# Kernel optimization log

Measured on AMD Instinct MI355X. Metric: run time of the kernel, lower is better.

The kernel has to match this reference:

```python
import jax, jax.numpy as jnp
import numpy as np

B, T, HID = 8, 4, 2048
H, HKV, D = 32, 8, 64   # query heads, kv heads, head_dim
S = 8192                # cached kv length
EPS = 1e-6
SCALE = D ** -0.5


def _rmsnorm(x, w, eps=EPS):
    xf = x.astype(jnp.float32)
    var = jnp.mean(xf * xf, axis=-1, keepdims=True)
    return w * (xf * jax.lax.rsqrt(var + eps)).astype(x.dtype)


def _rotate_half(x):
    half = x.shape[-1] // 2
    return jnp.concatenate([-x[..., half:], x[..., :half]], axis=-1)


def setup_inputs() -> dict:
    key = jax.random.key(0)
    ks = jax.random.split(key, 12)
    f = jnp.float32
    x = jax.random.normal(ks[0], (B, T, HID), f)
    theta = jax.random.uniform(ks[1], (B, T, D), f, 0.0, 2.0 * np.pi)
    cos = jnp.cos(theta)
    sin = jnp.sin(theta)
    cache_keys = jax.random.normal(ks[2], (B, HKV, S, D), f) * 0.5
    cache_values = jax.random.normal(ks[3], (B, HKV, S, D), f) * 0.5
    wq = jax.random.normal(ks[4], (HID, H * D), f) * 0.02
    wk = jax.random.normal(ks[5], (HID, HKV * D), f) * 0.02
    wv = jax.random.normal(ks[6], (HID, HKV * D), f) * 0.02
    wo = jax.random.normal(ks[7], (H * D, HID), f) * 0.02
    q_norm_w = jnp.ones((D,), f)
    k_norm_w = jnp.ones((D,), f)
    return {"x": x, "cos": cos, "sin": sin, "cache_keys": cache_keys,
            "cache_values": cache_values, "wq": wq, "wk": wk, "wv": wv,
            "wo": wo, "q_norm_w": q_norm_w, "k_norm_w": k_norm_w}


def reference(x, cos, sin, cache_keys, cache_values, wq, wk, wv, wo, q_norm_w, k_norm_w):
    b, t, _ = x.shape
    # projections + per-head RMSNorm on q/k -> [B,H,T,D]
    q = _rmsnorm((x @ wq).reshape(b, t, H, D), q_norm_w).transpose(0, 2, 1, 3)
    k = _rmsnorm((x @ wk).reshape(b, t, HKV, D), k_norm_w).transpose(0, 2, 1, 3)
    v = (x @ wv).reshape(b, t, HKV, D).transpose(0, 2, 1, 3)
    # RoPE (GPT-NeoX style), cos/sin broadcast over heads
    c = cos[:, None]  # [B,1,T,D]
    s = sin[:, None]
    q = q * c + _rotate_half(q) * s
    k = k * c + _rotate_half(k) * s
    # KV-cache concat along seq dim
    k_full = jnp.concatenate([cache_keys, k], axis=2)   # [B,HKV,S+T,D]
    v_full = jnp.concatenate([cache_values, v], axis=2)
    # GQA attention without materializing repeated KV heads:
    n_rep = H // HKV
    qg = q.reshape(b, HKV, n_rep, t, D)                 # [B,G,R,T,D]
    scores = jnp.einsum('bgrtd,bgsd->bgrts', qg, k_full) * SCALE
    p = jax.nn.softmax(scores, axis=-1)                 # cache present -> no causal mask
    og = jnp.einsum('bgrts,bgsd->bgrtd', p, v_full)
    out = og.reshape(b, H, t, D).transpose(0, 2, 1, 3).reshape(b, t, H * D) @ wo
    return (out, k_full, v_full)
```

## Files before the change

### kernel.cpp

```cpp
#include <hip/hip_runtime.h>
#include <math.h>

#define B 8
#define T 4
#define HID 2048
#define H 32
#define HKV 8
#define D 64
#define S 8192
#define ST (S + T)
#define NREP (H / HKV)
#define EPS 1e-6f
#define SCALE 0.125f

#define SCB 256
#define NSUB 4
#define SUB 64
#define NCB 33
#define NCAT 3072

typedef __attribute__((ext_vector_type(8))) _Float16 half8;
typedef __attribute__((ext_vector_type(4))) _Float16 half4;
typedef __attribute__((ext_vector_type(4))) float f32x4;

#define LGKM_BARRIER()                                                   \
    do {                                                                 \
        asm volatile("s_waitcnt lgkmcnt(0)" ::: "memory");               \
        __builtin_amdgcn_s_barrier();                                    \
        __builtin_amdgcn_sched_barrier(0);                               \
    } while (0)

static __device__ __forceinline__ half8 cvt8(const float4 a, const float4 b) {
    half8 f;
    f[0] = (_Float16)a.x; f[1] = (_Float16)a.y; f[2] = (_Float16)a.z; f[3] = (_Float16)a.w;
    f[4] = (_Float16)b.x; f[5] = (_Float16)b.y; f[6] = (_Float16)b.z; f[7] = (_Float16)b.w;
    return f;
}
static __device__ __forceinline__ half4 cvt4v(const f32x4 a) {
    half4 f;
    f[0] = (_Float16)a[0]; f[1] = (_Float16)a[1]; f[2] = (_Float16)a[2]; f[3] = (_Float16)a[3];
    return f;
}

__global__ __launch_bounds__(256) void gemm_qkv_mfma(const float* __restrict__ x,
                                                     const float* __restrict__ wq,
                                                     const float* __restrict__ wk,
                                                     const float* __restrict__ wv,
                                                     float* __restrict__ part) {
    __shared__ __align__(16) _Float16 xs[32][136];
    __shared__ __align__(16) _Float16 wsl[32][136];

    const int tid = threadIdx.x;
    const int lane = tid & 63;
    const int w = tid >> 6;
    const int q16 = lane & 15;
    const int kgrp = lane >> 4;
    const int tile = blockIdx.x;
    const int ky = blockIdx.y;
    const int kbase = ky * 1024;

    const float* wsrc; int N, lcbase;
    if (tile < 64)      { wsrc = wq; N = 2048; lcbase = tile * 32; }
    else if (tile < 80) { wsrc = wk; N = 512;  lcbase = (tile - 64) * 32; }
    else                { wsrc = wv; N = 512;  lcbase = (tile - 80) * 32; }

    const int r0 = (w >> 1) * 16, c0 = (w & 1) * 16;
    f32x4 acc = {0.f, 0.f, 0.f, 0.f};

    for (int kc = 0; kc < 8; ++kc) {
        const int k0 = kbase + kc * 128;
#pragma unroll
        for (int i = 0; i < 4; ++i) {
            const int idx = tid + i * 256;
            const int m = idx >> 5, slot = idx & 31;
            const f32x4 xv = *(const f32x4*)&x[(size_t)m * HID + k0 + slot * 4];
            *(half4*)&xs[m][slot * 4] = cvt4v(xv);
        }
#pragma unroll
        for (int i = 0; i < 4; ++i) {
            const int idx = tid + i * 256;
            const int kk = idx >> 3, c4 = idx & 7;
            const f32x4 wv4 = *(const f32x4*)&wsrc[(size_t)(k0 + kk) * N + lcbase + c4 * 4];
            wsl[c4 * 4 + 0][kk] = (_Float16)wv4[0];
            wsl[c4 * 4 + 1][kk] = (_Float16)wv4[1];
            wsl[c4 * 4 + 2][kk] = (_Float16)wv4[2];
            wsl[c4 * 4 + 3][kk] = (_Float16)wv4[3];
        }
        __syncthreads();
#pragma unroll
        for (int ks = 0; ks < 4; ++ks) {
            const half8 af = *(const half8*)&xs[r0 + q16][ks * 32 + kgrp * 8];
            const half8 bf = *(const half8*)&wsl[c0 + q16][ks * 32 + kgrp * 8];
            acc = __builtin_amdgcn_mfma_f32_16x16x32_f16(af, bf, acc, 0, 0, 0);
        }
        __syncthreads();
    }

    const int gcol = tile * 32 + c0 + q16;
#pragma unroll
    for (int r = 0; r < 4; ++r) {
        const int m = r0 + kgrp * 4 + r;
        part[((size_t)ky * 32 + m) * NCAT + gcol] = acc[r];
    }
}

__global__ __launch_bounds__(256) void gemm_out_mfma(const float* __restrict__ og,
                                                     const float* __restrict__ wo,
                                                     float* __restrict__ out) {
    __shared__ __align__(16) _Float16 xs[32][136];
    __shared__ __align__(16) _Float16 wsl[32][136];

    const int tid = threadIdx.x;
    const int lane = tid & 63;
    const int w = tid >> 6;
    const int q16 = lane & 15;
    const int kgrp = lane >> 4;
    const int tile = blockIdx.x;
    const int ky = blockIdx.y;
    const int kbase = ky * 1024;
    const int lcbase = tile * 32;

    const int r0 = (w >> 1) * 16, c0 = (w & 1) * 16;
    f32x4 acc = {0.f, 0.f, 0.f, 0.f};

    for (int kc = 0; kc < 8; ++kc) {
        const int k0 = kbase + kc * 128;
#pragma unroll
        for (int i = 0; i < 4; ++i) {
            const int idx = tid + i * 256;
            const int m = idx >> 5, slot = idx & 31;
            const f32x4 xv = *(const f32x4*)&og[(size_t)m * 2048 + k0 + slot * 4];
            *(half4*)&xs[m][slot * 4] = cvt4v(xv);
        }
#pragma unroll
        for (int i = 0; i < 4; ++i) {
            const int idx = tid + i * 256;
            const int kk = idx >> 3, c4 = idx & 7;
            const f32x4 wv4 = *(const f32x4*)&wo[(size_t)(k0 + kk) * 2048 + lcbase + c4 * 4];
            wsl[c4 * 4 + 0][kk] = (_Float16)wv4[0];
            wsl[c4 * 4 + 1][kk] = (_Float16)wv4[1];
            wsl[c4 * 4 + 2][kk] = (_Float16)wv4[2];
            wsl[c4 * 4 + 3][kk] = (_Float16)wv4[3];
        }
        __syncthreads();
#pragma unroll
        for (int ks = 0; ks < 4; ++ks) {
            const half8 af = *(const half8*)&xs[r0 + q16][ks * 32 + kgrp * 8];
            const half8 bf = *(const half8*)&wsl[c0 + q16][ks * 32 + kgrp * 8];
            acc = __builtin_amdgcn_mfma_f32_16x16x32_f16(af, bf, acc, 0, 0, 0);
        }
        __syncthreads();
    }

    const int gcol = lcbase + c0 + q16;
#pragma unroll
    for (int r = 0; r < 4; ++r) {
        const int m = r0 + kgrp * 4 + r;
        atomicAdd(&out[(size_t)m * 2048 + gcol], acc[r]);
    }
}

__global__ __launch_bounds__(256) void qkv_post(const float* __restrict__ part,
                                                const float* __restrict__ cosb,
                                                const float* __restrict__ sinb,
                                                const float* __restrict__ qnw,
                                                const float* __restrict__ knw,
                                                float* __restrict__ q_fin,
                                                float* __restrict__ kfull,
                                                float* __restrict__ vfull) {
    const int wid = (blockIdx.x * 256 + threadIdx.x) >> 6;
    const int lane = threadIdx.x & 63;
    if (wid < 1024) {
        const int m = wid >> 5, h = wid & 31;
        const size_t c = (size_t)m * NCAT + h * 64 + lane;
        float v = part[c] + part[c + (size_t)32 * NCAT];
        float ss = v * v;
#pragma unroll
        for (int off = 32; off; off >>= 1) ss += __shfl_xor(ss, off);
        float nv = qnw[lane] * v * rsqrtf(ss * (1.f / 64.f) + EPS);
        float other = __shfl_xor(nv, 32);
        float rot = (lane < 32) ? -other : other;
        float outv = nv * cosb[m * 64 + lane] + rot * sinb[m * 64 + lane];
        q_fin[(size_t)m * 2048 + h * 64 + lane] = outv * SCALE;
    } else if (wid < 1280) {
        const int idx = wid - 1024;
        const int m = idx >> 3, g = idx & 7;
        const size_t c = (size_t)m * NCAT + 2048 + g * 64 + lane;
        float v = part[c] + part[c + (size_t)32 * NCAT];
        float ss = v * v;
#pragma unroll
        for (int off = 32; off; off >>= 1) ss += __shfl_xor(ss, off);
        float nv = knw[lane] * v * rsqrtf(ss * (1.f / 64.f) + EPS);
        float other = __shfl_xor(nv, 32);
        float rot = (lane < 32) ? -other : other;
        float outv = nv * cosb[m * 64 + lane] + rot * sinb[m * 64 + lane];
        const int b = m >> 2, t = m & 3;
        kfull[((size_t)(b * HKV + g) * ST + S + t) * D + lane] = outv;
    } else if (wid < 1536) {
        const int idx = wid - 1280;
        const int m = idx >> 3, g = idx & 7;
        const size_t c = (size_t)m * NCAT + 2560 + g * 64 + lane;
        float v = part[c] + part[c + (size_t)32 * NCAT];
        const int b = m >> 2, t = m & 3;
        vfull[((size_t)(b * HKV + g) * ST + S + t) * D + lane] = v;
    }
}

__global__ __launch_bounds__(256, 5) void attn_part(const float* __restrict__ q_fin,
                                                    const float* __restrict__ ck,
                                                    const float* __restrict__ cv,
                                                    float* __restrict__ kfull,
                                                    float* __restrict__ vfull,
                                                    float* __restrict__ o_part,
                                                    float* __restrict__ ml_part) {
    const int bg = blockIdx.x;
    const int cb = blockIdx.y;
    const int b = bg >> 3, g = bg & 7;
    const int tid = threadIdx.x;
    const int lane = tid & 63;
    const int w = tid >> 6;
    const int q16 = lane & 15;
    const int kgrp = lane >> 4;

    __shared__ __align__(16) _Float16 kl[SUB][72];
    __shared__ __align__(16) _Float16 vl[SUB][72];
    __shared__ __align__(16) float scs[16][68];
    __shared__ __align__(16) _Float16 pb[16][72];
    __shared__ float Mrun[16], Lrun[16], srow[16];

    const bool full = (cb < 32);
    const int vm1 = full ? (SUB - 1) : (ST - S - 1);

    if (tid < 16) { Mrun[tid] = -3e38f; Lrun[tid] = 0.f; }

    half8 qf[2];
    {
        const float* qp = q_fin + ((size_t)(b * T + (q16 & 3)) * H + g * NREP + (q16 >> 2)) * D;
#pragma unroll
        for (int h = 0; h < 2; ++h) {
            const float* p = qp + h * 32 + kgrp * 8;
            qf[h] = cvt8(*(const float4*)p, *(const float4*)(p + 4));
        }
    }

    f32x4 oacc = {0.f, 0.f, 0.f, 0.f};
    const int dglob = w * 16 + q16;

    if (full) {
        const f32x4* ksrc = (const f32x4*)(ck + ((size_t)bg * S + (size_t)cb * SCB) * D);
        const f32x4* vsrc = (const f32x4*)(cv + ((size_t)bg * S + (size_t)cb * SCB) * D);
        f32x4* kdst = (f32x4*)(kfull + ((size_t)bg * ST + (size_t)cb * SCB) * D);
        f32x4* vdst = (f32x4*)(vfull + ((size_t)bg * ST + (size_t)cb * SCB) * D);

        f32x4 kr[4], vr[4];
#pragma unroll
        for (int i = 0; i < 4; ++i) {
            kr[i] = __builtin_nontemporal_load(&ksrc[tid + i * 256]);
            vr[i] = __builtin_nontemporal_load(&vsrc[tid + i * 256]);
        }

#pragma unroll
        for (int su = 0; su < NSUB; ++su) {
#pragma unroll
            for (int i = 0; i < 4; ++i) {
                const int idx = tid + i * 256;
                __builtin_nontemporal_store(kr[i], &kdst[su * 1024 + idx]);
                __builtin_nontemporal_store(vr[i], &vdst[su * 1024 + idx]);
                const int r = idx >> 4, cg = idx & 15;
                *(half4*)&kl[r][cg * 4] = cvt4v(kr[i]);
                *(half4*)&vl[r][cg * 4] = cvt4v(vr[i]);
            }
            if (su < NSUB - 1) {
#pragma unroll
                for (int i = 0; i < 4; ++i) {
                    kr[i] = __builtin_nontemporal_load(&ksrc[(su + 1) * 1024 + tid + i * 256]);
                    vr[i] = __builtin_nontemporal_load(&vsrc[(su + 1) * 1024 + tid + i * 256]);
                }
            }
            LGKM_BARRIER();

            {
                const int sl = w * 16 + q16;
                f32x4 acc = {0.f, 0.f, 0.f, 0.f};
#pragma unroll
                for (int h = 0; h < 2; ++h) {
                    const half8 kf = *(const half8*)&kl[sl][h * 32 + kgrp * 8];
                    acc = __builtin_amdgcn_mfma_f32_16x16x32_f16(kf, qf[h], acc, 0, 0, 0);
                }
                *(f32x4*)&scs[q16][w * 16 + kgrp * 4] = acc;
            }
            LGKM_BARRIER();

#pragma unroll
            for (int rr = 0; rr < 4; ++rr) {
                const int row = w * 4 + rr;
                const float v = scs[row][lane];
                float m_ = v;
#pragma unroll
                for (int off = 32; off; off >>= 1) m_ = fmaxf(m_, __shfl_xor(m_, off));
                const float Mold = Mrun[row];
                const float Mnew = fmaxf(Mold, m_);
                const float e = __expf(v - Mnew);
                float l = e;
#pragma unroll
                for (int off = 32; off; off >>= 1) l += __shfl_xor(l, off);
                pb[row][lane] = (_Float16)e;
                if (lane == 0) {
                    const float sc_ = __expf(Mold - Mnew);
                    srow[row] = sc_;
                    Lrun[row] = Lrun[row] * sc_ + l;
                    Mrun[row] = Mnew;
                }
            }
            LGKM_BARRIER();

            {
#pragma unroll
                for (int r = 0; r < 4; ++r) oacc[r] *= srow[kgrp * 4 + r];
#pragma unroll
                for (int ks = 0; ks < 2; ++ks) {
                    const half8 pa = *(const half8*)&pb[q16][ks * 32 + kgrp * 8];
                    half8 vf;
#pragma unroll
                    for (int e = 0; e < 8; ++e) {
                        vf[e] = vl[ks * 32 + kgrp * 8 + e][dglob];
                    }
                    oacc = __builtin_amdgcn_mfma_f32_16x16x32_f16(pa, vf, oacc, 0, 0, 0);
                }
            }
            LGKM_BARRIER();
        }
    } else {
        if (tid < 64) {
            const int r = tid >> 4, cg = tid & 15;
            const int rc = min(r, vm1);
            const f32x4 k4 = *(const f32x4*)(kfull + ((size_t)bg * ST + S + rc) * D + cg * 4);
            const f32x4 v4 = *(const f32x4*)(vfull + ((size_t)bg * ST + S + rc) * D + cg * 4);
            *(half4*)&kl[r][cg * 4] = cvt4v(k4);
            *(half4*)&vl[r][cg * 4] = cvt4v(v4);
        }
        __syncthreads();

        {
            const int sl = min(w * 16 + q16, vm1);
            f32x4 acc = {0.f, 0.f, 0.f, 0.f};
#pragma unroll
            for (int h = 0; h < 2; ++h) {
                const half8 kf = *(const half8*)&kl[sl][h * 32 + kgrp * 8];
                acc = __builtin_amdgcn_mfma_f32_16x16x32_f16(kf, qf[h], acc, 0, 0, 0);
            }
            const int sbase = w * 16 + kgrp * 4;
#pragma unroll
            for (int r = 0; r < 4; ++r)
                scs[q16][sbase + r] = (sbase + r <= vm1) ? acc[r] : -1e30f;
        }
        __syncthreads();

#pragma unroll
        for (int rr = 0; rr < 4; ++rr) {
            const int row = w * 4 + rr;
            const float v = scs[row][lane];
            float m_ = v;
#pragma unroll
            for (int off = 32; off; off >>= 1) m_ = fmaxf(m_, __shfl_xor(m_, off));
            const float Mnew = m_;
            const float e = __expf(v - Mnew);
            float l = e;
#pragma unroll
            for (int off = 32; off; off >>= 1) l += __shfl_xor(l, off);
            pb[row][lane] = (_Float16)e;
            if (lane == 0) { srow[row] = 0.f; Lrun[row] = l; Mrun[row] = Mnew; }
        }
        __syncthreads();

        {
#pragma unroll
            for (int ks = 0; ks < 2; ++ks) {
                const half8 pa = *(const half8*)&pb[q16][ks * 32 + kgrp * 8];
                half8 vf;
#pragma unroll
                for (int e = 0; e < 8; ++e) {
                    const int sr = min(ks * 32 + kgrp * 8 + e, vm1);
                    vf[e] = vl[sr][dglob];
                }
                oacc = __builtin_amdgcn_mfma_f32_16x16x32_f16(pa, vf, oacc, 0, 0, 0);
            }
        }
        __syncthreads();
    }

#pragma unroll
    for (int r = 0; r < 4; ++r) {
        const int row = kgrp * 4 + r;
        o_part[(((size_t)bg * 16 + row) * NCB + cb) * 64 + dglob] = oacc[r];
    }
    if (tid < 16) {
        ml_part[(((size_t)bg * 16 + tid) * NCB + cb) * 2 + 0] = Mrun[tid];
        ml_part[(((size_t)bg * 16 + tid) * NCB + cb) * 2 + 1] = Lrun[tid];
    }
}

__global__ __launch_bounds__(256) void attn_combine(const float* __restrict__ o_part,
                                                    const float* __restrict__ ml_part,
                                                    float* __restrict__ og,
                                                    float* __restrict__ out) {
    out[blockIdx.x * 256 + threadIdx.x] = 0.f;

    const int gw = (blockIdx.x * 256 + threadIdx.x) >> 6;
    const int lane = threadIdx.x & 63;
    const int bg = gw >> 4, row = gw & 15;
    float M = -1e30f, L = 0.f, O = 0.f;
    for (int c = 0; c < NCB; ++c) {
        const float m_ = ml_part[((size_t)gw * NCB + c) * 2 + 0];
        const float l_ = ml_part[((size_t)gw * NCB + c) * 2 + 1];
        const float o_ = o_part[((size_t)gw * NCB + c) * 64 + lane];
        const float Mn = fmaxf(M, m_);
        const float fa = __expf(M - Mn), fb = __expf(m_ - Mn);
        O = O * fa + o_ * fb;
        L = L * fa + l_ * fb;
        M = Mn;
    }
    const float o = O / L;
    const int b = bg >> 3, g = bg & 7, r = row >> 2, t = row & 3;
    og[((size_t)(b * T + t) * H + (g * NREP + r)) * D + lane] = o;
}

extern "C" void kernel_launch(void* const* d_in, const int* in_sizes, int n_in,
                              void* d_out, int out_size, void* d_ws, size_t ws_size,
                              hipStream_t stream) {
    const float* x    = (const float*)d_in[0];
    const float* cosb = (const float*)d_in[1];
    const float* sinb = (const float*)d_in[2];
    const float* ck   = (const float*)d_in[3];
    const float* cv   = (const float*)d_in[4];
    const float* wq   = (const float*)d_in[5];
    const float* wk   = (const float*)d_in[6];
    const float* wvp  = (const float*)d_in[7];
    const float* wo   = (const float*)d_in[8];
    const float* qnw  = (const float*)d_in[9];
    const float* knw  = (const float*)d_in[10];

    float* out   = (float*)d_out;
    float* kfull = out + 65536;
    float* vfull = kfull + (size_t)B * HKV * ST * D;

    float* ws      = (float*)d_ws;
    float* qkvp    = ws;
    float* q_fin   = qkvp + (size_t)2 * 32 * NCAT;
    float* og      = q_fin + 65536;
    float* o_part  = og + 65536;
    float* ml_part = o_part + (size_t)64 * 16 * NCB * 64;

    gemm_qkv_mfma<<<dim3(96, 2), 256, 0, stream>>>(x, wq, wk, wvp, qkvp);

    qkv_post<<<384, 256, 0, stream>>>(qkvp, cosb, sinb, qnw, knw, q_fin, kfull, vfull);

    attn_part<<<dim3(64, NCB), 256, 0, stream>>>(q_fin, ck, cv, kfull, vfull, o_part, ml_part);

    attn_combine<<<256, 256, 0, stream>>>(o_part, ml_part, og, out);

    gemm_out_mfma<<<dim3(64, 2), 256, 0, stream>>>(og, wo, out);
}
```

Baseline: 150.6 us.

## Fuse QKV post-processing into attention kernel and raise GEMM split-K to eight

Removes the separate qkv_post kernel. Each attention block now reduces the split-K partials itself and applies RMSNorm and RoPE to its query fragments, and the tail block also builds and writes the new K/V rows. The KV cache loads are issued before the q preparation so their latency overlaps with it. Split-K for both projection GEMMs goes from 2 to 8 to give more parallel blocks, at the cost of more partial-sum reads, redundant q normalization across the 33 chunk blocks, and more atomics in the output GEMM.

```diff
diff --git a/kernel.cpp b/kernel.cpp
--- a/kernel.cpp
+++ b/kernel.cpp
@@ -18,6 +18,7 @@
 #define SUB 64
 #define NCB 33
 #define NCAT 3072
+#define KSPL 8
 
 typedef __attribute__((ext_vector_type(8))) _Float16 half8;
 typedef __attribute__((ext_vector_type(4))) _Float16 half4;
@@ -30,12 +31,6 @@
         __builtin_amdgcn_sched_barrier(0);                               \
     } while (0)
 
-static __device__ __forceinline__ half8 cvt8(const float4 a, const float4 b) {
-    half8 f;
-    f[0] = (_Float16)a.x; f[1] = (_Float16)a.y; f[2] = (_Float16)a.z; f[3] = (_Float16)a.w;
-    f[4] = (_Float16)b.x; f[5] = (_Float16)b.y; f[6] = (_Float16)b.z; f[7] = (_Float16)b.w;
-    return f;
-}
 static __device__ __forceinline__ half4 cvt4v(const f32x4 a) {
     half4 f;
     f[0] = (_Float16)a[0]; f[1] = (_Float16)a[1]; f[2] = (_Float16)a[2]; f[3] = (_Float16)a[3];
@@ -57,7 +52,7 @@
     const int kgrp = lane >> 4;
     const int tile = blockIdx.x;
     const int ky = blockIdx.y;
-    const int kbase = ky * 1024;
+    const int kbase = ky * (HID / KSPL);
 
     const float* wsrc; int N, lcbase;
     if (tile < 64)      { wsrc = wq; N = 2048; lcbase = tile * 32; }
@@ -67,7 +62,7 @@
     const int r0 = (w >> 1) * 16, c0 = (w & 1) * 16;
     f32x4 acc = {0.f, 0.f, 0.f, 0.f};
 
-    for (int kc = 0; kc < 8; ++kc) {
+    for (int kc = 0; kc < 2; ++kc) {
         const int k0 = kbase + kc * 128;
 #pragma unroll
         for (int i = 0; i < 4; ++i) {
@@ -117,13 +112,13 @@
     const int kgrp = lane >> 4;
     const int tile = blockIdx.x;
     const int ky = blockIdx.y;
-    const int kbase = ky * 1024;
+    const int kbase = ky * (HID / KSPL);
     const int lcbase = tile * 32;
 
     const int r0 = (w >> 1) * 16, c0 = (w & 1) * 16;
     f32x4 acc = {0.f, 0.f, 0.f, 0.f};
 
-    for (int kc = 0; kc < 8; ++kc) {
+    for (int kc = 0; kc < 2; ++kc) {
         const int k0 = kbase + kc * 128;
 #pragma unroll
         for (int i = 0; i < 4; ++i) {
@@ -160,53 +155,11 @@
     }
 }
 
-__global__ __launch_bounds__(256) void qkv_post(const float* __restrict__ part,
-                                                const float* __restrict__ cosb,
-                                                const float* __restrict__ sinb,
-                                                const float* __restrict__ qnw,
-                                                const float* __restrict__ knw,
-                                                float* __restrict__ q_fin,
-                                                float* __restrict__ kfull,
-                                                float* __restrict__ vfull) {
-    const int wid = (blockIdx.x * 256 + threadIdx.x) >> 6;
-    const int lane = threadIdx.x & 63;
-    if (wid < 1024) {
-        const int m = wid >> 5, h = wid & 31;
-        const size_t c = (size_t)m * NCAT + h * 64 + lane;
-        float v = part[c] + part[c + (size_t)32 * NCAT];
-        float ss = v * v;
-#pragma unroll
-        for (int off = 32; off; off >>= 1) ss += __shfl_xor(ss, off);
-        float nv = qnw[lane] * v * rsqrtf(ss * (1.f / 64.f) + EPS);
-        float other = __shfl_xor(nv, 32);
-        float rot = (lane < 32) ? -other : other;
-        float outv = nv * cosb[m * 64 + lane] + rot * sinb[m * 64 + lane];
-        q_fin[(size_t)m * 2048 + h * 64 + lane] = outv * SCALE;
-    } else if (wid < 1280) {
-        const int idx = wid - 1024;
-        const int m = idx >> 3, g = idx & 7;
-        const size_t c = (size_t)m * NCAT + 2048 + g * 64 + lane;
-        float v = part[c] + part[c + (size_t)32 * NCAT];
-        float ss = v * v;
-#pragma unroll
-        for (int off = 32; off; off >>= 1) ss += __shfl_xor(ss, off);
-        float nv = knw[lane] * v * rsqrtf(ss * (1.f / 64.f) + EPS);
-        float other = __shfl_xor(nv, 32);
-        float rot = (lane < 32) ? -other : other;
-        float outv = nv * cosb[m * 64 + lane] + rot * sinb[m * 64 + lane];
-        const int b = m >> 2, t = m & 3;
-        kfull[((size_t)(b * HKV + g) * ST + S + t) * D + lane] = outv;
-    } else if (wid < 1536) {
-        const int idx = wid - 1280;
-        const int m = idx >> 3, g = idx & 7;
-        const size_t c = (size_t)m * NCAT + 2560 + g * 64 + lane;
-        float v = part[c] + part[c + (size_t)32 * NCAT];
-        const int b = m >> 2, t = m & 3;
-        vfull[((size_t)(b * HKV + g) * ST + S + t) * D + lane] = v;
-    }
-}
-
-__global__ __launch_bounds__(256, 5) void attn_part(const float* __restrict__ q_fin,
+__global__ __launch_bounds__(256, 5) void attn_part(const float* __restrict__ part,
+                                                    const float* __restrict__ cosb,
+                                                    const float* __restrict__ sinb,
+                                                    const float* __restrict__ qnw,
+                                                    const float* __restrict__ knw,
                                                     const float* __restrict__ ck,
                                                     const float* __restrict__ cv,
                                                     float* __restrict__ kfull,
@@ -233,31 +186,61 @@
 
     if (tid < 16) { Mrun[tid] = -3e38f; Lrun[tid] = 0.f; }
 
-    half8 qf[2];
-    {
-        const float* qp = q_fin + ((size_t)(b * T + (q16 & 3)) * H + g * NREP + (q16 >> 2)) * D;
-#pragma unroll
-        for (int h = 0; h < 2; ++h) {
-            const float* p = qp + h * 32 + kgrp * 8;
-            qf[h] = cvt8(*(const float4*)p, *(const float4*)(p + 4));
-        }
-    }
-
-    f32x4 oacc = {0.f, 0.f, 0.f, 0.f};
-    const int dglob = w * 16 + q16;
-
+    const f32x4* ksrc = (const f32x4*)(ck + ((size_t)bg * S + (size_t)cb * SCB) * D);
+    const f32x4* vsrc = (const f32x4*)(cv + ((size_t)bg * S + (size_t)cb * SCB) * D);
+    f32x4 kr[4], vr[4];
     if (full) {
-        const f32x4* ksrc = (const f32x4*)(ck + ((size_t)bg * S + (size_t)cb * SCB) * D);
-        const f32x4* vsrc = (const f32x4*)(cv + ((size_t)bg * S + (size_t)cb * SCB) * D);
-        f32x4* kdst = (f32x4*)(kfull + ((size_t)bg * ST + (size_t)cb * SCB) * D);
-        f32x4* vdst = (f32x4*)(vfull + ((size_t)bg * ST + (size_t)cb * SCB) * D);
-
-        f32x4 kr[4], vr[4];
 #pragma unroll
         for (int i = 0; i < 4; ++i) {
             kr[i] = __builtin_nontemporal_load(&ksrc[tid + i * 256]);
             vr[i] = __builtin_nontemporal_load(&vsrc[tid + i * 256]);
         }
+    }
+
+    half8 qf[2];
+    {
+        const int t = q16 & 3, r = q16 >> 2;
+        const int m = b * T + t;
+        const int h = g * NREP + r;
+        const int d0 = kgrp * 8;
+        float v0[8], v1[8];
+#pragma unroll
+        for (int e = 0; e < 8; ++e) { v0[e] = 0.f; v1[e] = 0.f; }
+#pragma unroll
+        for (int p = 0; p < KSPL; ++p) {
+            const float* bp = part + ((size_t)p * 32 + m) * NCAT + h * 64 + d0;
+            const f32x4 a0 = *(const f32x4*)bp, a1 = *(const f32x4*)(bp + 4);
+            const f32x4 b0 = *(const f32x4*)(bp + 32), b1 = *(const f32x4*)(bp + 36);
+#pragma unroll
+            for (int e = 0; e < 4; ++e) {
+                v0[e] += a0[e]; v0[e + 4] += a1[e];
+                v1[e] += b0[e]; v1[e + 4] += b1[e];
+            }
+        }
+        float ss = 0.f;
+#pragma unroll
+        for (int e = 0; e < 8; ++e) ss += v0[e] * v0[e] + v1[e] * v1[e];
+        ss += __shfl_xor(ss, 16);
+        ss += __shfl_xor(ss, 32);
+        const float rn = rsqrtf(ss * (1.f / 64.f) + EPS);
+#pragma unroll
+        for (int e = 0; e < 8; ++e) {
+            const int dA = d0 + e, dB = 32 + d0 + e;
+            const float nv0 = qnw[dA] * v0[e] * rn;
+            const float nv1 = qnw[dB] * v1[e] * rn;
+            const float o0 = nv0 * cosb[m * 64 + dA] - nv1 * sinb[m * 64 + dA];
+            const float o1 = nv1 * cosb[m * 64 + dB] + nv0 * sinb[m * 64 + dB];
+            qf[0][e] = (_Float16)(o0 * SCALE);
+            qf[1][e] = (_Float16)(o1 * SCALE);
+        }
+    }
+
+    f32x4 oacc = {0.f, 0.f, 0.f, 0.f};
+    const int dglob = w * 16 + q16;
+
+    if (full) {
+        f32x4* kdst = (f32x4*)(kfull + ((size_t)bg * ST + (size_t)cb * SCB) * D);
+        f32x4* vdst = (f32x4*)(vfull + ((size_t)bg * ST + (size_t)cb * SCB) * D);
 
 #pragma unroll
         for (int su = 0; su < NSUB; ++su) {
@@ -331,13 +314,25 @@
             LGKM_BARRIER();
         }
     } else {
-        if (tid < 64) {
-            const int r = tid >> 4, cg = tid & 15;
-            const int rc = min(r, vm1);
-            const f32x4 k4 = *(const f32x4*)(kfull + ((size_t)bg * ST + S + rc) * D + cg * 4);
-            const f32x4 v4 = *(const f32x4*)(vfull + ((size_t)bg * ST + S + rc) * D + cg * 4);
-            *(half4*)&kl[r][cg * 4] = cvt4v(k4);
-            *(half4*)&vl[r][cg * 4] = cvt4v(v4);
+        {
+            const int m = b * T + w;
+            float kv_ = 0.f, vv_ = 0.f;
+#pragma unroll
+            for (int p = 0; p < KSPL; ++p) {
+                kv_ += part[((size_t)p * 32 + m) * NCAT + 2048 + g * 64 + lane];
+                vv_ += part[((size_t)p * 32 + m) * NCAT + 2560 + g * 64 + lane];
+            }
+            float ss = kv_ * kv_;
+#pragma unroll
+            for (int off = 32; off; off >>= 1) ss += __shfl_xor(ss, off);
+            const float nv = knw[lane] * kv_ * rsqrtf(ss * (1.f / 64.f) + EPS);
+            const float other = __shfl_xor(nv, 32);
+            const float rot = (lane < 32) ? -other : other;
+            const float outv = nv * cosb[m * 64 + lane] + rot * sinb[m * 64 + lane];
+            kfull[((size_t)(b * HKV + g) * ST + S + w) * D + lane] = outv;
+            vfull[((size_t)(b * HKV + g) * ST + S + w) * D + lane] = vv_;
+            kl[w][lane] = (_Float16)outv;
+            vl[w][lane] = (_Float16)vv_;
         }
         __syncthreads();
 
@@ -369,7 +364,7 @@
 #pragma unroll
             for (int off = 32; off; off >>= 1) l += __shfl_xor(l, off);
             pb[row][lane] = (_Float16)e;
-            if (lane == 0) { srow[row] = 0.f; Lrun[row] = l; Mrun[row] = Mnew; }
+            if (lane == 0) { Lrun[row] = l; Mrun[row] = Mnew; }
         }
         __syncthreads();
 
@@ -446,18 +441,16 @@
 
     float* ws      = (float*)d_ws;
     float* qkvp    = ws;
-    float* q_fin   = qkvp + (size_t)2 * 32 * NCAT;
-    float* og      = q_fin + 65536;
+    float* og      = qkvp + (size_t)KSPL * 32 * NCAT;
     float* o_part  = og + 65536;
     float* ml_part = o_part + (size_t)64 * 16 * NCB * 64;
 
-    gemm_qkv_mfma<<<dim3(96, 2), 256, 0, stream>>>(x, wq, wk, wvp, qkvp);
-
-    qkv_post<<<384, 256, 0, stream>>>(qkvp, cosb, sinb, qnw, knw, q_fin, kfull, vfull);
-
-    attn_part<<<dim3(64, NCB), 256, 0, stream>>>(q_fin, ck, cv, kfull, vfull, o_part, ml_part);
+    gemm_qkv_mfma<<<dim3(96, KSPL), 256, 0, stream>>>(x, wq, wk, wvp, qkvp);
+
+    attn_part<<<dim3(64, NCB), 256, 0, stream>>>(qkvp, cosb, sinb, qnw, knw,
+                                                 ck, cv, kfull, vfull, o_part, ml_part);
 
     attn_combine<<<256, 256, 0, stream>>>(o_part, ml_part, og, out);
 
-    gemm_out_mfma<<<dim3(64, 2), 256, 0, stream>>>(og, wo, out);
-}
+    gemm_out_mfma<<<dim3(64, KSPL), 256, 0, stream>>>(og, wo, out);
+}
```

After: 155.0 us. 1.03x slower.
